# Optimization experiments

Hardware: AMD Instinct MI355X
Metric: run time of the kernel (lower is better)

The kernel has to match this reference:

```python
import jax, jax.numpy as jnp
import numpy as np
import itertools

B, H, W, C = 64, 28, 28, 576
NH, WS = 18, 7
KD = C // NH          # head dim = 32 (attn_ratio=1 so d == key_dim)
HID = 4 * C           # mlp hidden
N = WS * WS           # tokens per window = 49


def _bias_idxs():
    points = list(itertools.product(range(WS), range(WS)))
    offsets, idxs = {}, []
    for p1 in points:
        for p2 in points:
            off = (abs(p1[0] - p2[0]), abs(p1[1] - p2[1]))
            if off not in offsets:
                offsets[off] = len(offsets)
            idxs.append(offsets[off])
    return np.asarray(idxs, dtype=np.int64).reshape(N, N), len(offsets)


def setup_inputs() -> dict:
    key = jax.random.key(0)
    ks = jax.random.split(key, 10)
    idxs, n_off = _bias_idxs()  # n_off == 49
    s = 0.02
    return {
        "x": jax.random.normal(ks[0], (B, H * W, C), jnp.float32),
        "gamma_a": jnp.ones((C,), jnp.float32),
        "beta_a": jnp.zeros((C,), jnp.float32),
        "qkv_w": jax.random.normal(ks[1], (3 * C, C), jnp.float32) * s,
        "qkv_b": jnp.zeros((3 * C,), jnp.float32),
        "proj_w": jax.random.normal(ks[2], (C, C), jnp.float32) * s,
        "proj_b": jnp.zeros((C,), jnp.float32),
        "attn_biases": jax.random.normal(ks[3], (NH, n_off), jnp.float32) * s,
        "conv_w": jax.random.normal(ks[4], (C, 1, 3, 3), jnp.float32) * 0.1,
        "bn_gamma": jnp.ones((C,), jnp.float32),
        "bn_beta": jnp.zeros((C,), jnp.float32),
        "bn_mean": jnp.zeros((C,), jnp.float32),
        "bn_var": jax.random.uniform(ks[5], (C,), jnp.float32, 0.5, 1.5),
        "gamma_m": jnp.ones((C,), jnp.float32),
        "beta_m": jnp.zeros((C,), jnp.float32),
        "fc1_w": jax.random.normal(ks[6], (HID, C), jnp.float32) * s,
        "fc1_b": jnp.zeros((HID,), jnp.float32),
        "fc2_w": jax.random.normal(ks[7], (C, HID), jnp.float32) * s,
        "fc2_b": jnp.zeros((C,), jnp.float32),
        "bias_idxs": jnp.asarray(idxs),
    }


def _ln(x, g, b, eps=1e-5):
    mu = x.mean(-1, keepdims=True)
    var = ((x - mu) ** 2).mean(-1, keepdims=True)
    return (x - mu) * jax.lax.rsqrt(var + eps) * g + b


def reference(x, gamma_a, beta_a, qkv_w, qkv_b, proj_w, proj_b, attn_biases,
              conv_w, bn_gamma, bn_beta, bn_mean, bn_var,
              gamma_m, beta_m, fc1_w, fc1_b, fc2_w, fc2_b, bias_idxs):
    scale = KD ** -0.5
    nWh, nWw = H // WS, W // WS
    res = x
    # ---- window partition: (B, H*W, C) -> (B*nWh*nWw, 49, C) ----
    xw = x.reshape(B, nWh, WS, nWw, WS, C).transpose(0, 1, 3, 2, 4, 5)
    xw = xw.reshape(-1, N, C)
    # ---- windowed attention with gathered relative-position bias ----
    h = _ln(xw, gamma_a, beta_a)
    qkv = h @ qkv_w.T + qkv_b                       # (Bw, N, 3C)
    qkv = qkv.reshape(-1, N, NH, 3 * KD)
    q, k, v = jnp.split(qkv, 3, axis=-1)            # each (Bw, N, NH, KD)
    q = q.transpose(0, 2, 1, 3)
    k = k.transpose(0, 2, 1, 3)
    v = v.transpose(0, 2, 1, 3)
    bias = attn_biases[:, bias_idxs]                # (NH, N, N)
    attn = jnp.einsum('bhnd,bhmd->bhnm', q, k) * scale + bias
    attn = jax.nn.softmax(attn, axis=-1)
    out = jnp.einsum('bhnm,bhmd->bhnd', attn, v)    # (Bw, NH, N, KD)
    out = out.transpose(0, 2, 1, 3).reshape(-1, N, C) @ proj_w.T + proj_b
    # ---- window reverse ----
    out = out.reshape(B, nWh, nWw, WS, WS, C).transpose(0, 1, 3, 2, 4, 5)
    out = out.reshape(B, H * W, C)
    x = res + out
    # ---- depthwise 3x3 conv + BatchNorm (inference stats) ----
    xc = x.transpose(0, 2, 1).reshape(B, C, H, W)
    xc = jax.lax.conv_general_dilated(
        xc, conv_w, (1, 1), [(1, 1), (1, 1)],
        feature_group_count=C,
        dimension_numbers=('NCHW', 'OIHW', 'NCHW'))
    eps = 1e-5
    inv = (jax.lax.rsqrt(bn_var + eps) * bn_gamma)[:, None, None]
    xc = (xc - bn_mean[:, None, None]) * inv + bn_beta[:, None, None]
    x = xc.reshape(B, C, H * W).transpose(0, 2, 1)
    # ---- MLP with pre-LayerNorm ----
    hm = _ln(x, gamma_m, beta_m)
    hm = jax.nn.gelu(hm @ fc1_w.T + fc1_b, approximate=False)
    hm = hm @ fc2_w.T + fc2_b
    return x + hm
```

## Files before the change

kernel.cpp:

```cpp
#include <hip/hip_runtime.h>
#include <hip/hip_bf16.h>

typedef __bf16 v8bf  __attribute__((ext_vector_type(8)));
typedef __bf16 v4bf  __attribute__((ext_vector_type(4)));
typedef float  f32x4 __attribute__((ext_vector_type(4)));
typedef float  f32x8 __attribute__((ext_vector_type(8)));

#define TOKENS 50176
#define CDIM   576
#define NHEAD  18
#define QKVD   1728

__device__ __forceinline__ void gld16(const __bf16* g, __bf16* l)
{
    __builtin_amdgcn_global_load_lds(
        (const __attribute__((address_space(1))) void*)g,
        (__attribute__((address_space(3))) void*)l,
        16, 0, 0);
}

__device__ __forceinline__ float fast_gelu(float x)
{
    const float z  = x * 0.70710678118654752f;
    const float az = fabsf(z);
    const float t  = __frcp_rn(1.0f + 0.3275911f * az);
    float p = 1.061405429f;
    p = p * t - 1.453152027f;
    p = p * t + 1.421413741f;
    p = p * t - 0.284496736f;
    p = p * t + 0.254829592f;
    const float e   = __expf(-z * z);
    float erfv = 1.0f - p * t * e;
    erfv = copysignf(erfv, z);
    return 0.5f * x * (1.0f + erfv);
}

__global__ __launch_bounds__(256)
void cast_kernel(const float* __restrict__ in, __bf16* __restrict__ out)
{
    const size_t i = ((size_t)blockIdx.x * 256 + threadIdx.x) * 4;
    f32x4 v = *(const f32x4*)&in[i];
    v4bf o;
#pragma unroll
    for (int j = 0; j < 4; ++j) o[j] = (__bf16)v[j];
    *(v4bf*)&out[i] = o;
}

__global__ __launch_bounds__(64)
void conv_prep(const float* __restrict__ w, const float* __restrict__ bg,
               const float* __restrict__ bb, const float* __restrict__ bm,
               const float* __restrict__ bv, __bf16* __restrict__ wt,
               float* __restrict__ bias2)
{
    const int c = blockIdx.x * 64 + threadIdx.x;
    const float inv = rsqrtf(bv[c] + 1e-5f) * bg[c];
#pragma unroll
    for (int t = 0; t < 9; ++t) wt[t * CDIM + c] = (__bf16)(w[c * 9 + t] * inv);
    bias2[c] = bb[c] - bm[c] * inv;
}

template<typename InT>
__global__ __launch_bounds__(256)
void ln_kernel(const InT* __restrict__ x, const float* __restrict__ g,
               const float* __restrict__ b, __bf16* __restrict__ out)
{
    const int lane = threadIdx.x & 63;
    const int wid  = threadIdx.x >> 6;
    const size_t t = (size_t)blockIdx.x * 4 + wid;
    const InT* row = x + t * CDIM;

    float v[16];
    float sum = 0.f, sq = 0.f;
    if constexpr (sizeof(InT) == 2) {
        v8bf d0 = *(const v8bf*)&row[(size_t)lane * 8];
#pragma unroll
        for (int j = 0; j < 8; ++j) { float f = (float)d0[j]; v[j] = f; sum += f; sq += f * f; }
    } else {
        f32x8 d0 = *(const f32x8*)&row[(size_t)lane * 8];
#pragma unroll
        for (int j = 0; j < 8; ++j) { float f = d0[j]; v[j] = f; sum += f; sq += f * f; }
    }
    if (lane < 8) {
        if constexpr (sizeof(InT) == 2) {
            v8bf d1 = *(const v8bf*)&row[(size_t)(lane + 64) * 8];
#pragma unroll
            for (int j = 0; j < 8; ++j) { float f = (float)d1[j]; v[8 + j] = f; sum += f; sq += f * f; }
        } else {
            f32x8 d1 = *(const f32x8*)&row[(size_t)(lane + 64) * 8];
#pragma unroll
            for (int j = 0; j < 8; ++j) { float f = d1[j]; v[8 + j] = f; sum += f; sq += f * f; }
        }
    }
#pragma unroll
    for (int o = 32; o >= 1; o >>= 1) {
        sum += __shfl_xor(sum, o, 64);
        sq  += __shfl_xor(sq,  o, 64);
    }
    const float mean = sum * (1.0f / CDIM);
    const float rstd = rsqrtf(sq * (1.0f / CDIM) - mean * mean + 1e-5f);

    {
        int c0 = lane * 8;
        v8bf o0;
#pragma unroll
        for (int j = 0; j < 8; ++j)
            o0[j] = (__bf16)((v[j] - mean) * rstd * g[c0 + j] + b[c0 + j]);
        *(v8bf*)&out[t * CDIM + c0] = o0;
    }
    if (lane < 8) {
        int c0 = (lane + 64) * 8;
        v8bf o1;
#pragma unroll
        for (int j = 0; j < 8; ++j)
            o1[j] = (__bf16)((v[8 + j] - mean) * rstd * g[c0 + j] + b[c0 + j]);
        *(v8bf*)&out[t * CDIM + c0] = o1;
    }
}

template<int EPI, typename OutT, typename AddT>
__global__ __launch_bounds__(512, 1)
void gemm_bt(const __bf16* __restrict__ A, const __bf16* __restrict__ W,
             const float* __restrict__ bias, const AddT* __restrict__ add,
             OutT* __restrict__ C, int N, int K, int nN)
{
    constexpr int BM = 256, BN = 192, BK = 32;
    constexpr int ASZ = BM * BK;
    constexpr int BSZ = BN * BK;
    __shared__ __bf16 L[4][ASZ + BSZ];
    const int tid = threadIdx.x, lane = tid & 63, wid = tid >> 6;
    const int lr = lane & 15, kh = lane >> 4;
    const int wm = wid >> 2, wn = wid & 3;

    const int nwg = gridDim.x, bid = blockIdx.x;
    const int q = nwg >> 3, r = nwg & 7;
    const int xcd = bid & 7, jc = bid >> 3;
    const int wgid = (xcd < r ? xcd * (q + 1) : r * (q + 1) + (xcd - r) * q) + jc;
    const int mblk = wgid / nN, nblk = wgid - mblk * nN;
    const int m0 = mblk * BM, n0 = nblk * BN;

    const __bf16* pA = A + (size_t)(m0 + wid * 32 + lr) * K + kh * 8;
    const __bf16* pW = W + (size_t)(n0 + (wid < 6 ? wid : 0) * 32 + lr) * K + kh * 8;

    auto stageA = [&](int s, int kt) {
#pragma unroll
        for (int i = 0; i < 2; ++i)
            gld16(pA + (size_t)(i * 16) * K + kt * BK, &L[s][(wid * 2 + i) * 512]);
    };
    auto stageB = [&](int s, int kt) {
        if (wid < 6) {
#pragma unroll
            for (int i = 0; i < 2; ++i)
                gld16(pW + (size_t)(i * 16) * K + kt * BK,
                      &L[s][ASZ + (wid * 2 + i) * 512]);
        }
    };

    const int off = lane * 8;

    f32x4 acc[8][3] = {};
    const int NT = K / BK;

    stageA(0, 0); stageB(0, 0);
    stageA(1, 1); stageB(1, 1);

    for (int t = 0; t < NT; ++t) {
        if (t + 1 < NT) {
            if (wid < 6) asm volatile("s_waitcnt vmcnt(4)" ::: "memory");
            else         asm volatile("s_waitcnt vmcnt(2)" ::: "memory");
        } else {
            asm volatile("s_waitcnt vmcnt(0)" ::: "memory");
        }
        __builtin_amdgcn_s_barrier();

        const __bf16* Ls = L[t & 3];
        v8bf bfr[3], afr[4];

#pragma unroll
        for (int nf = 0; nf < 3; ++nf)
            bfr[nf] = *(const v8bf*)&Ls[ASZ + (wn * 3 + nf) * 512 + off];
#pragma unroll
        for (int mf = 0; mf < 4; ++mf)
            afr[mf] = *(const v8bf*)&Ls[(wm * 8 + mf) * 512 + off];

        if (t + 2 < NT) stageA((t + 2) & 3, t + 2);

        __builtin_amdgcn_s_setprio(1);
#pragma unroll
        for (int mf = 0; mf < 4; ++mf)
#pragma unroll
            for (int nf = 0; nf < 3; ++nf)
                acc[mf][nf] = __builtin_amdgcn_mfma_f32_16x16x32_bf16(
                    afr[mf], bfr[nf], acc[mf][nf], 0, 0, 0);
        __builtin_amdgcn_s_setprio(0);
        __builtin_amdgcn_s_barrier();

#pragma unroll
        for (int mf = 0; mf < 4; ++mf)
            afr[mf] = *(const v8bf*)&Ls[(wm * 8 + 4 + mf) * 512 + off];

        if (t + 2 < NT) stageB((t + 2) & 3, t + 2);

        __builtin_amdgcn_s_setprio(1);
#pragma unroll
        for (int mf = 0; mf < 4; ++mf)
#pragma unroll
            for (int nf = 0; nf < 3; ++nf)
                acc[4 + mf][nf] = __builtin_amdgcn_mfma_f32_16x16x32_bf16(
                    afr[mf], bfr[nf], acc[4 + mf][nf], 0, 0, 0);
        __builtin_amdgcn_s_setprio(0);
    }

#pragma unroll
    for (int mf = 0; mf < 8; ++mf)
#pragma unroll
        for (int nf = 0; nf < 3; ++nf)
#pragma unroll
            for (int rr = 0; rr < 4; ++rr) {
                int row = m0 + wm * 128 + mf * 16 + kh * 4 + rr;
                int col = n0 + wn * 48 + nf * 16 + lr;
                float vv = acc[mf][nf][rr] + bias[col];
                if (EPI == 1) vv += (float)add[(size_t)row * N + col];
                if (EPI == 2) vv = fast_gelu(vv);
                C[(size_t)row * N + col] = (OutT)vv;
            }
}

__global__ __launch_bounds__(64)
void attn_kernel(const __bf16* __restrict__ qkv, const float* __restrict__ biases,
                 const int* __restrict__ bidx, __bf16* __restrict__ out)
{
    const int head = blockIdx.x;
    const int win  = blockIdx.y;
    const int tid  = threadIdx.x;
    const int b  = win >> 4;
    const int wy = (win >> 2) & 3;
    const int wx = win & 3;
    __shared__ float kk[49][32];
    __shared__ float vv[49][32];
    const size_t hb = (size_t)head * 96;

    for (int e = tid; e < 49 * 32; e += 64) {
        int n = e >> 5, d = e & 31;
        int iy = n / 7, ix = n - iy * 7;
        size_t t = (size_t)b * 784 + (size_t)(wy * 7 + iy) * 28 + wx * 7 + ix;
        const __bf16* p = qkv + t * QKVD + hb;
        kk[n][d] = (float)p[32 + d];
        vv[n][d] = (float)p[64 + d];
    }
    float q[32];
    size_t tmine = 0;
    if (tid < 49) {
        int iy = tid / 7, ix = tid - iy * 7;
        tmine = (size_t)b * 784 + (size_t)(wy * 7 + iy) * 28 + wx * 7 + ix;
        const __bf16* p = qkv + tmine * QKVD + hb;
#pragma unroll
        for (int d = 0; d < 32; ++d) q[d] = (float)p[d];
    }
    __syncthreads();
    if (tid >= 49) return;

    const float scale = 0.17677669529663687f;
    float s[49];
    float mx = -1e30f;
    const int*   brow = bidx + tid * 49;
    const float* bh   = biases + head * 49;
#pragma unroll
    for (int m = 0; m < 49; ++m) {
        float dot = 0.f;
#pragma unroll
        for (int d = 0; d < 32; ++d) dot += q[d] * kk[m][d];
        float val = dot * scale + bh[brow[m]];
        s[m] = val;
        mx = fmaxf(mx, val);
    }
    float sum = 0.f;
#pragma unroll
    for (int m = 0; m < 49; ++m) { float e = __expf(s[m] - mx); s[m] = e; sum += e; }
    const float rs = 1.0f / sum;

    __bf16* op = out + tmine * CDIM + (size_t)head * 32;
#pragma unroll
    for (int d = 0; d < 32; ++d) {
        float a = 0.f;
#pragma unroll
        for (int m = 0; m < 49; ++m) a += s[m] * vv[m][d];
        op[d] = (__bf16)(a * rs);
    }
}

__global__ __launch_bounds__(256)
void conv_bn_v(const __bf16* __restrict__ xin, const __bf16* __restrict__ wt,
               const float* __restrict__ bias2, __bf16* __restrict__ xout)
{
    const size_t gt = (size_t)blockIdx.x * 256 + threadIdx.x;
    const int g = (int)(gt % 72);
    const size_t p = gt / 72;
    const int bimg = (int)(p / 784);
    const int pix  = (int)(p - (size_t)bimg * 784);
    const int y = pix / 28, xx = pix - y * 28;
    const int c0 = g * 8;

    float acc[8];
    {
        f32x4 b0 = *(const f32x4*)&bias2[c0];
        f32x4 b1 = *(const f32x4*)&bias2[c0 + 4];
#pragma unroll
        for (int jj = 0; jj < 4; ++jj) { acc[jj] = b0[jj]; acc[4 + jj] = b1[jj]; }
    }
#pragma unroll
    for (int dy = 0; dy < 3; ++dy) {
        int ny = y + dy - 1;
        if (ny < 0 || ny >= 28) continue;
#pragma unroll
        for (int dx = 0; dx < 3; ++dx) {
            int nx = xx + dx - 1;
            if (nx < 0 || nx >= 28) continue;
            v8bf xv = *(const v8bf*)&xin[((size_t)bimg * 784 + ny * 28 + nx) * CDIM + c0];
            v8bf wv = *(const v8bf*)&wt[(dy * 3 + dx) * CDIM + c0];
#pragma unroll
            for (int jj = 0; jj < 8; ++jj) acc[jj] += (float)xv[jj] * (float)wv[jj];
        }
    }
    v8bf o;
#pragma unroll
    for (int jj = 0; jj < 8; ++jj) o[jj] = (__bf16)acc[jj];
    *(v8bf*)&xout[p * CDIM + c0] = o;
}

extern "C" void kernel_launch(void* const* d_in, const int* in_sizes, int n_in,
                              void* d_out, int out_size, void* d_ws, size_t ws_size,
                              hipStream_t stream)
{
    (void)in_sizes; (void)n_in; (void)out_size; (void)ws_size;
    const float* x          = (const float*)d_in[0];
    const float* gamma_a    = (const float*)d_in[1];
    const float* beta_a     = (const float*)d_in[2];
    const float* qkv_w      = (const float*)d_in[3];
    const float* qkv_b      = (const float*)d_in[4];
    const float* proj_w     = (const float*)d_in[5];
    const float* proj_b     = (const float*)d_in[6];
    const float* attn_bias  = (const float*)d_in[7];
    const float* conv_w     = (const float*)d_in[8];
    const float* bn_g       = (const float*)d_in[9];
    const float* bn_b       = (const float*)d_in[10];
    const float* bn_m       = (const float*)d_in[11];
    const float* bn_v       = (const float*)d_in[12];
    const float* gamma_m    = (const float*)d_in[13];
    const float* beta_m     = (const float*)d_in[14];
    const float* fc1_w      = (const float*)d_in[15];
    const float* fc1_b      = (const float*)d_in[16];
    const float* fc2_w      = (const float*)d_in[17];
    const float* fc2_b      = (const float*)d_in[18];
    const int*   bidx       = (const int*)d_in[19];

    const size_t T = TOKENS;
    __bf16* ws     = (__bf16*)d_ws;
    __bf16* hbuf   = ws;
    __bf16* qkvbuf = ws + T * 576;
    __bf16* aout   = ws;
    __bf16* x2     = ws + T * 2304;
    __bf16* x3     = x2 + T * 576;
    __bf16* lnm    = x2;
    __bf16* f1     = ws;
    __bf16* wq     = x3 + T * 576;
    __bf16* wp     = wq + (size_t)QKVD * CDIM;
    __bf16* w1     = wp + (size_t)CDIM * CDIM;
    __bf16* w2     = w1 + (size_t)2304 * CDIM;
    __bf16* wt     = w2 + (size_t)CDIM * 2304;
    float*  bias2  = (float*)(wt + 9 * CDIM);
    float*  outp   = (float*)d_out;

    cast_kernel<<<dim3((QKVD * CDIM) / 1024), 256, 0, stream>>>(qkv_w, wq);
    cast_kernel<<<dim3((CDIM * CDIM) / 1024), 256, 0, stream>>>(proj_w, wp);
    cast_kernel<<<dim3((2304 * CDIM) / 1024), 256, 0, stream>>>(fc1_w, w1);
    cast_kernel<<<dim3((CDIM * 2304) / 1024), 256, 0, stream>>>(fc2_w, w2);
    conv_prep<<<dim3(9), 64, 0, stream>>>(conv_w, bn_g, bn_b, bn_m, bn_v, wt, bias2);

    ln_kernel<float><<<dim3(T / 4), 256, 0, stream>>>(x, gamma_a, beta_a, hbuf);
    gemm_bt<0, __bf16, float><<<dim3(196 * 9), 512, 0, stream>>>(
        hbuf, wq, qkv_b, nullptr, qkvbuf, QKVD, CDIM, 9);
    attn_kernel<<<dim3(NHEAD, 1024), 64, 0, stream>>>(qkvbuf, attn_bias, bidx, aout);
    gemm_bt<1, __bf16, float><<<dim3(196 * 3), 512, 0, stream>>>(
        aout, wp, proj_b, x, x2, CDIM, CDIM, 3);
    conv_bn_v<<<dim3(14112), 256, 0, stream>>>(x2, wt, bias2, x3);
    ln_kernel<__bf16><<<dim3(T / 4), 256, 0, stream>>>(x3, gamma_m, beta_m, lnm);
    gemm_bt<2, __bf16, float><<<dim3(196 * 12), 512, 0, stream>>>(
        lnm, w1, fc1_b, nullptr, f1, 2304, CDIM, 12);
    gemm_bt<1, float, __bf16><<<dim3(196 * 3), 512, 0, stream>>>(
        f1, w2, fc2_b, x3, outp, CDIM, 2304, 3);
}
```

Baseline: 1.021 ms.

## Rework GEMM to 4-wave 32x32x16 MFMA tiles with double buffering

Rewrites the shared GEMM kernel to use 256 threads (4 waves, 2x2 layout) with 32x32x16 bf16 MFMA instructions instead of 8 waves with 16x16x32, each wave now covering a 128x96 subtile. The LDS pipeline shrinks from a 4-stage to a 2-stage buffer with a full vmcnt(0) wait and barrier per k-step, and launch bounds allow two workgroups per CU. The aim is a higher MFMA-to-LDS-read ratio and better occupancy. The trade-off is a shallower prefetch that may expose global load latency, plus different register pressure.

```diff
diff --git a/kernel.cpp b/kernel.cpp
--- a/kernel.cpp
+++ b/kernel.cpp
@@ -5,6 +5,7 @@
 typedef __bf16 v4bf  __attribute__((ext_vector_type(4)));
 typedef float  f32x4 __attribute__((ext_vector_type(4)));
 typedef float  f32x8 __attribute__((ext_vector_type(8)));
+typedef float  f32x16 __attribute__((ext_vector_type(16)));
 
 #define TOKENS 50176
 #define CDIM   576
@@ -118,111 +119,118 @@
 }
 
 template<int EPI, typename OutT, typename AddT>
-__global__ __launch_bounds__(512, 1)
+__global__ __launch_bounds__(256, 2)
 void gemm_bt(const __bf16* __restrict__ A, const __bf16* __restrict__ W,
              const float* __restrict__ bias, const AddT* __restrict__ add,
              OutT* __restrict__ C, int N, int K, int nN)
 {
-    constexpr int BM = 256, BN = 192, BK = 32;
-    constexpr int ASZ = BM * BK;
-    constexpr int BSZ = BN * BK;
-    __shared__ __bf16 L[4][ASZ + BSZ];
+    constexpr int BK = 32;
+    constexpr int ASZ = 256 * BK;
+    constexpr int BSZ = 192 * BK;
+    __shared__ __bf16 L[2][ASZ + BSZ];
     const int tid = threadIdx.x, lane = tid & 63, wid = tid >> 6;
-    const int lr = lane & 15, kh = lane >> 4;
-    const int wm = wid >> 2, wn = wid & 3;
+    const int l31 = lane & 31, kg = lane >> 5;
+    const int wm = wid >> 1, wn = wid & 1;
 
     const int nwg = gridDim.x, bid = blockIdx.x;
     const int q = nwg >> 3, r = nwg & 7;
     const int xcd = bid & 7, jc = bid >> 3;
     const int wgid = (xcd < r ? xcd * (q + 1) : r * (q + 1) + (xcd - r) * q) + jc;
     const int mblk = wgid / nN, nblk = wgid - mblk * nN;
-    const int m0 = mblk * BM, n0 = nblk * BN;
-
-    const __bf16* pA = A + (size_t)(m0 + wid * 32 + lr) * K + kh * 8;
-    const __bf16* pW = W + (size_t)(n0 + (wid < 6 ? wid : 0) * 32 + lr) * K + kh * 8;
-
-    auto stageA = [&](int s, int kt) {
-#pragma unroll
-        for (int i = 0; i < 2; ++i)
-            gld16(pA + (size_t)(i * 16) * K + kt * BK, &L[s][(wid * 2 + i) * 512]);
+    const int m0 = mblk * 256, n0 = nblk * 192;
+
+    const __bf16* pAl = A + (size_t)(m0 + l31) * K + kg * 8;
+    const __bf16* pWl = W + (size_t)(n0 + l31) * K + kg * 8;
+
+    auto stage = [&](int s, int kt) {
+        const int kk = kt * BK;
+#pragma unroll
+        for (int i = 0; i < 7; ++i) {
+            const int e = wid + 4 * i;
+            if (e < 16) {
+                gld16(pAl + (size_t)((e >> 1) * 32) * K + kk + (e & 1) * 16,
+                      &L[s][e * 512]);
+            } else {
+                const int e2 = e - 16;
+                gld16(pWl + (size_t)((e2 >> 1) * 32) * K + kk + (e2 & 1) * 16,
+                      &L[s][ASZ + e2 * 512]);
+            }
+        }
     };
-    auto stageB = [&](int s, int kt) {
-        if (wid < 6) {
-#pragma unroll
-            for (int i = 0; i < 2; ++i)
-                gld16(pW + (size_t)(i * 16) * K + kt * BK,
-                      &L[s][ASZ + (wid * 2 + i) * 512]);
-        }
-    };
-
-    const int off = lane * 8;
-
-    f32x4 acc[8][3] = {};
+
+    const int lo = lane * 8;
+
+    f32x16 acc[4][3] = {};
     const int NT = K / BK;
 
-    stageA(0, 0); stageB(0, 0);
-    stageA(1, 1); stageB(1, 1);
-
+    stage(0, 0);
+    asm volatile("s_waitcnt vmcnt(0)" ::: "memory");
+    __builtin_amdgcn_s_barrier();
+
+    int cur = 0;
     for (int t = 0; t < NT; ++t) {
+        const __bf16* Ls = L[cur];
+        v8bf a0[4], b0[3];
+#pragma unroll
+        for (int mf = 0; mf < 4; ++mf)
+            a0[mf] = *(const v8bf*)&Ls[((wm * 4 + mf) * 2 + 0) * 512 + lo];
+#pragma unroll
+        for (int nf = 0; nf < 3; ++nf)
+            b0[nf] = *(const v8bf*)&Ls[ASZ + ((wn * 3 + nf) * 2 + 0) * 512 + lo];
+
+        if (t + 1 < NT) stage(cur ^ 1, t + 1);
+
+        __builtin_amdgcn_s_setprio(1);
+#pragma unroll
+        for (int mf = 0; mf < 4; ++mf)
+#pragma unroll
+            for (int nf = 0; nf < 3; ++nf)
+                acc[mf][nf] = __builtin_amdgcn_mfma_f32_32x32x16_bf16(
+                    a0[mf], b0[nf], acc[mf][nf], 0, 0, 0);
+        __builtin_amdgcn_s_setprio(0);
+
+        v8bf a1[4], b1[3];
+#pragma unroll
+        for (int mf = 0; mf < 4; ++mf)
+            a1[mf] = *(const v8bf*)&Ls[((wm * 4 + mf) * 2 + 1) * 512 + lo];
+#pragma unroll
+        for (int nf = 0; nf < 3; ++nf)
+            b1[nf] = *(const v8bf*)&Ls[ASZ + ((wn * 3 + nf) * 2 + 1) * 512 + lo];
+
+        __builtin_amdgcn_s_setprio(1);
+#pragma unroll
+        for (int mf = 0; mf < 4; ++mf)
+#pragma unroll
+            for (int nf = 0; nf < 3; ++nf)
+                acc[mf][nf] = __builtin_amdgcn_mfma_f32_32x32x16_bf16(
+                    a1[mf], b1[nf], acc[mf][nf], 0, 0, 0);
+        __builtin_amdgcn_s_setprio(0);
+
         if (t + 1 < NT) {
-            if (wid < 6) asm volatile("s_waitcnt vmcnt(4)" ::: "memory");
-            else         asm volatile("s_waitcnt vmcnt(2)" ::: "memory");
-        } else {
             asm volatile("s_waitcnt vmcnt(0)" ::: "memory");
-        }
-        __builtin_amdgcn_s_barrier();
-
-        const __bf16* Ls = L[t & 3];
-        v8bf bfr[3], afr[4];
-
-#pragma unroll
-        for (int nf = 0; nf < 3; ++nf)
-            bfr[nf] = *(const v8bf*)&Ls[ASZ + (wn * 3 + nf) * 512 + off];
-#pragma unroll
-        for (int mf = 0; mf < 4; ++mf)
-            afr[mf] = *(const v8bf*)&Ls[(wm * 8 + mf) * 512 + off];
-
-        if (t + 2 < NT) stageA((t + 2) & 3, t + 2);
-
-        __builtin_amdgcn_s_setprio(1);
-#pragma unroll
-        for (int mf = 0; mf < 4; ++mf)
-#pragma unroll
-            for (int nf = 0; nf < 3; ++nf)
-                acc[mf][nf] = __builtin_amdgcn_mfma_f32_16x16x32_bf16(
-                    afr[mf], bfr[nf], acc[mf][nf], 0, 0, 0);
-        __builtin_amdgcn_s_setprio(0);
-        __builtin_amdgcn_s_barrier();
-
-#pragma unroll
-        for (int mf = 0; mf < 4; ++mf)
-            afr[mf] = *(const v8bf*)&Ls[(wm * 8 + 4 + mf) * 512 + off];
-
-        if (t + 2 < NT) stageB((t + 2) & 3, t + 2);
-
-        __builtin_amdgcn_s_setprio(1);
-#pragma unroll
-        for (int mf = 0; mf < 4; ++mf)
-#pragma unroll
-            for (int nf = 0; nf < 3; ++nf)
-                acc[4 + mf][nf] = __builtin_amdgcn_mfma_f32_16x16x32_bf16(
-                    afr[mf], bfr[nf], acc[4 + mf][nf], 0, 0, 0);
-        __builtin_amdgcn_s_setprio(0);
-    }
-
-#pragma unroll
-    for (int mf = 0; mf < 8; ++mf)
-#pragma unroll
-        for (int nf = 0; nf < 3; ++nf)
-#pragma unroll
-            for (int rr = 0; rr < 4; ++rr) {
-                int row = m0 + wm * 128 + mf * 16 + kh * 4 + rr;
-                int col = n0 + wn * 48 + nf * 16 + lr;
-                float vv = acc[mf][nf][rr] + bias[col];
+            __builtin_amdgcn_s_barrier();
+            cur ^= 1;
+        }
+    }
+
+    float bc[3];
+#pragma unroll
+    for (int nf = 0; nf < 3; ++nf) bc[nf] = bias[n0 + wn * 96 + nf * 32 + l31];
+
+#pragma unroll
+    for (int mf = 0; mf < 4; ++mf)
+#pragma unroll
+        for (int nf = 0; nf < 3; ++nf) {
+            const int col = n0 + wn * 96 + nf * 32 + l31;
+#pragma unroll
+            for (int rr = 0; rr < 16; ++rr) {
+                const int row = m0 + wm * 128 + mf * 32 + (rr & 3) + 8 * (rr >> 2) + 4 * kg;
+                float vv = acc[mf][nf][rr] + bc[nf];
                 if (EPI == 1) vv += (float)add[(size_t)row * N + col];
                 if (EPI == 2) vv = fast_gelu(vv);
                 C[(size_t)row * N + col] = (OutT)vv;
             }
+        }
 }
 
 __global__ __launch_bounds__(64)
@@ -377,15 +385,15 @@
     conv_prep<<<dim3(9), 64, 0, stream>>>(conv_w, bn_g, bn_b, bn_m, bn_v, wt, bias2);
 
     ln_kernel<float><<<dim3(T / 4), 256, 0, stream>>>(x, gamma_a, beta_a, hbuf);
-    gemm_bt<0, __bf16, float><<<dim3(196 * 9), 512, 0, stream>>>(
+    gemm_bt<0, __bf16, float><<<dim3(196 * 9), 256, 0, stream>>>(
         hbuf, wq, qkv_b, nullptr, qkvbuf, QKVD, CDIM, 9);
     attn_kernel<<<dim3(NHEAD, 1024), 64, 0, stream>>>(qkvbuf, attn_bias, bidx, aout);
-    gemm_bt<1, __bf16, float><<<dim3(196 * 3), 512, 0, stream>>>(
+    gemm_bt<1, __bf16, float><<<dim3(196 * 3), 256, 0, stream>>>(
         aout, wp, proj_b, x, x2, CDIM, CDIM, 3);
     conv_bn_v<<<dim3(14112), 256, 0, stream>>>(x2, wt, bias2, x3);
     ln_kernel<__bf16><<<dim3(T / 4), 256, 0, stream>>>(x3, gamma_m, beta_m, lnm);
-    gemm_bt<2, __bf16, float><<<dim3(196 * 12), 512, 0, stream>>>(
+    gemm_bt<2, __bf16, float><<<dim3(196 * 12), 256, 0, stream>>>(
         lnm, w1, fc1_b, nullptr, f1, 2304, CDIM, 12);
-    gemm_bt<1, float, __bf16><<<dim3(196 * 3), 512, 0, stream>>>(
+    gemm_bt<1, float, __bf16><<<dim3(196 * 3), 256, 0, stream>>>(
         f1, w2, fc2_b, x3, outp, CDIM, 2304, 3);
 }
```

New measurement: 1.023 ms. About the same (+0.1%).

## Fuse depthwise conv+BN with MLP LayerNorm; use 128-row tiles for N=576 GEMMs

Applied to the files above, without the earlier changes.

The depthwise conv+BN kernel now also computes the MLP pre-LayerNorm, one wavefront per token, and writes both the residual x3 and the normalized input in one pass. This removes a separate LN kernel launch and a full re-read of x3. The GEMM is templated on BM, and the proj and fc2 GEMMs (N=576, only 3 column tiles) use BM=128, doubling the grid from 588 to 1176 workgroups to fill the GPU better. The risks are a conv that is less parallel per thread and smaller tiles with less reuse per workgroup.

```diff
diff --git a/kernel.cpp b/kernel.cpp
--- a/kernel.cpp
+++ b/kernel.cpp
@@ -59,37 +59,26 @@
     bias2[c] = bb[c] - bm[c] * inv;
 }
 
-template<typename InT>
 __global__ __launch_bounds__(256)
-void ln_kernel(const InT* __restrict__ x, const float* __restrict__ g,
+void ln_kernel(const float* __restrict__ x, const float* __restrict__ g,
                const float* __restrict__ b, __bf16* __restrict__ out)
 {
     const int lane = threadIdx.x & 63;
     const int wid  = threadIdx.x >> 6;
     const size_t t = (size_t)blockIdx.x * 4 + wid;
-    const InT* row = x + t * CDIM;
+    const float* row = x + t * CDIM;
 
     float v[16];
     float sum = 0.f, sq = 0.f;
-    if constexpr (sizeof(InT) == 2) {
-        v8bf d0 = *(const v8bf*)&row[(size_t)lane * 8];
-#pragma unroll
-        for (int j = 0; j < 8; ++j) { float f = (float)d0[j]; v[j] = f; sum += f; sq += f * f; }
-    } else {
+    {
         f32x8 d0 = *(const f32x8*)&row[(size_t)lane * 8];
 #pragma unroll
         for (int j = 0; j < 8; ++j) { float f = d0[j]; v[j] = f; sum += f; sq += f * f; }
     }
     if (lane < 8) {
-        if constexpr (sizeof(InT) == 2) {
-            v8bf d1 = *(const v8bf*)&row[(size_t)(lane + 64) * 8];
-#pragma unroll
-            for (int j = 0; j < 8; ++j) { float f = (float)d1[j]; v[8 + j] = f; sum += f; sq += f * f; }
-        } else {
-            f32x8 d1 = *(const f32x8*)&row[(size_t)(lane + 64) * 8];
-#pragma unroll
-            for (int j = 0; j < 8; ++j) { float f = d1[j]; v[8 + j] = f; sum += f; sq += f * f; }
-        }
+        f32x8 d1 = *(const f32x8*)&row[(size_t)(lane + 64) * 8];
+#pragma unroll
+        for (int j = 0; j < 8; ++j) { float f = d1[j]; v[8 + j] = f; sum += f; sq += f * f; }
     }
 #pragma unroll
     for (int o = 32; o >= 1; o >>= 1) {
@@ -117,15 +106,17 @@
     }
 }
 
-template<int EPI, typename OutT, typename AddT>
+template<int BM, int EPI, typename OutT, typename AddT>
 __global__ __launch_bounds__(512, 1)
 void gemm_bt(const __bf16* __restrict__ A, const __bf16* __restrict__ W,
              const float* __restrict__ bias, const AddT* __restrict__ add,
              OutT* __restrict__ C, int N, int K, int nN)
 {
-    constexpr int BM = 256, BN = 192, BK = 32;
+    constexpr int BK  = 32;
     constexpr int ASZ = BM * BK;
-    constexpr int BSZ = BN * BK;
+    constexpr int BSZ = 192 * BK;
+    constexpr int MFR = BM / 32;
+    constexpr int MH  = MFR / 2;
     __shared__ __bf16 L[4][ASZ + BSZ];
     const int tid = threadIdx.x, lane = tid & 63, wid = tid >> 6;
     const int lr = lane & 15, kh = lane >> 4;
@@ -136,15 +127,21 @@
     const int xcd = bid & 7, jc = bid >> 3;
     const int wgid = (xcd < r ? xcd * (q + 1) : r * (q + 1) + (xcd - r) * q) + jc;
     const int mblk = wgid / nN, nblk = wgid - mblk * nN;
-    const int m0 = mblk * BM, n0 = nblk * BN;
-
-    const __bf16* pA = A + (size_t)(m0 + wid * 32 + lr) * K + kh * 8;
+    const int m0 = mblk * BM, n0 = nblk * 192;
+
+    const __bf16* pA;
+    if constexpr (BM == 256) pA = A + (size_t)(m0 + wid * 32 + lr) * K + kh * 8;
+    else                     pA = A + (size_t)(m0 + wid * 16 + lr) * K + kh * 8;
     const __bf16* pW = W + (size_t)(n0 + (wid < 6 ? wid : 0) * 32 + lr) * K + kh * 8;
 
     auto stageA = [&](int s, int kt) {
-#pragma unroll
-        for (int i = 0; i < 2; ++i)
-            gld16(pA + (size_t)(i * 16) * K + kt * BK, &L[s][(wid * 2 + i) * 512]);
+        if constexpr (BM == 256) {
+#pragma unroll
+            for (int i = 0; i < 2; ++i)
+                gld16(pA + (size_t)(i * 16) * K + kt * BK, &L[s][(wid * 2 + i) * 512]);
+        } else {
+            gld16(pA + kt * BK, &L[s][wid * 512]);
+        }
     };
     auto stageB = [&](int s, int kt) {
         if (wid < 6) {
@@ -155,9 +152,9 @@
         }
     };
 
-    const int off = lane * 8;
-
-    f32x4 acc[8][3] = {};
+    const int lo = lane * 8;
+
+    f32x4 acc[MFR][3] = {};
     const int NT = K / BK;
 
     stageA(0, 0); stageB(0, 0);
@@ -165,28 +162,33 @@
 
     for (int t = 0; t < NT; ++t) {
         if (t + 1 < NT) {
-            if (wid < 6) asm volatile("s_waitcnt vmcnt(4)" ::: "memory");
-            else         asm volatile("s_waitcnt vmcnt(2)" ::: "memory");
+            if constexpr (BM == 256) {
+                if (wid < 6) asm volatile("s_waitcnt vmcnt(4)" ::: "memory");
+                else         asm volatile("s_waitcnt vmcnt(2)" ::: "memory");
+            } else {
+                if (wid < 6) asm volatile("s_waitcnt vmcnt(3)" ::: "memory");
+                else         asm volatile("s_waitcnt vmcnt(1)" ::: "memory");
+            }
         } else {
             asm volatile("s_waitcnt vmcnt(0)" ::: "memory");
         }
         __builtin_amdgcn_s_barrier();
 
         const __bf16* Ls = L[t & 3];
-        v8bf bfr[3], afr[4];
+        v8bf bfr[3], afr[MH];
 
 #pragma unroll
         for (int nf = 0; nf < 3; ++nf)
-            bfr[nf] = *(const v8bf*)&Ls[ASZ + (wn * 3 + nf) * 512 + off];
-#pragma unroll
-        for (int mf = 0; mf < 4; ++mf)
-            afr[mf] = *(const v8bf*)&Ls[(wm * 8 + mf) * 512 + off];
+            bfr[nf] = *(const v8bf*)&Ls[ASZ + (wn * 3 + nf) * 512 + lo];
+#pragma unroll
+        for (int mf = 0; mf < MH; ++mf)
+            afr[mf] = *(const v8bf*)&Ls[(wm * MFR + mf) * 512 + lo];
 
         if (t + 2 < NT) stageA((t + 2) & 3, t + 2);
 
         __builtin_amdgcn_s_setprio(1);
 #pragma unroll
-        for (int mf = 0; mf < 4; ++mf)
+        for (int mf = 0; mf < MH; ++mf)
 #pragma unroll
             for (int nf = 0; nf < 3; ++nf)
                 acc[mf][nf] = __builtin_amdgcn_mfma_f32_16x16x32_bf16(
@@ -195,28 +197,28 @@
         __builtin_amdgcn_s_barrier();
 
 #pragma unroll
-        for (int mf = 0; mf < 4; ++mf)
-            afr[mf] = *(const v8bf*)&Ls[(wm * 8 + 4 + mf) * 512 + off];
+        for (int mf = 0; mf < MH; ++mf)
+            afr[mf] = *(const v8bf*)&Ls[(wm * MFR + MH + mf) * 512 + lo];
 
         if (t + 2 < NT) stageB((t + 2) & 3, t + 2);
 
         __builtin_amdgcn_s_setprio(1);
 #pragma unroll
-        for (int mf = 0; mf < 4; ++mf)
+        for (int mf = 0; mf < MH; ++mf)
 #pragma unroll
             for (int nf = 0; nf < 3; ++nf)
-                acc[4 + mf][nf] = __builtin_amdgcn_mfma_f32_16x16x32_bf16(
-                    afr[mf], bfr[nf], acc[4 + mf][nf], 0, 0, 0);
+                acc[MH + mf][nf] = __builtin_amdgcn_mfma_f32_16x16x32_bf16(
+                    afr[mf], bfr[nf], acc[MH + mf][nf], 0, 0, 0);
         __builtin_amdgcn_s_setprio(0);
     }
 
 #pragma unroll
-    for (int mf = 0; mf < 8; ++mf)
+    for (int mf = 0; mf < MFR; ++mf)
 #pragma unroll
         for (int nf = 0; nf < 3; ++nf)
 #pragma unroll
             for (int rr = 0; rr < 4; ++rr) {
-                int row = m0 + wm * 128 + mf * 16 + kh * 4 + rr;
+                int row = m0 + wm * (BM / 2) + mf * 16 + kh * 4 + rr;
                 int col = n0 + wn * 48 + nf * 16 + lr;
                 float vv = acc[mf][nf][rr] + bias[col];
                 if (EPI == 1) vv += (float)add[(size_t)row * N + col];
@@ -289,42 +291,101 @@
 }
 
 __global__ __launch_bounds__(256)
-void conv_bn_v(const __bf16* __restrict__ xin, const __bf16* __restrict__ wt,
-               const float* __restrict__ bias2, __bf16* __restrict__ xout)
-{
-    const size_t gt = (size_t)blockIdx.x * 256 + threadIdx.x;
-    const int g = (int)(gt % 72);
-    const size_t p = gt / 72;
+void conv_bn_ln(const __bf16* __restrict__ xin, const __bf16* __restrict__ wt,
+                const float* __restrict__ bias2, const float* __restrict__ g,
+                const float* __restrict__ b,
+                __bf16* __restrict__ x3, __bf16* __restrict__ lnm)
+{
+    const int lane = threadIdx.x & 63;
+    const int wid  = threadIdx.x >> 6;
+    const size_t p = (size_t)blockIdx.x * 4 + wid;
     const int bimg = (int)(p / 784);
     const int pix  = (int)(p - (size_t)bimg * 784);
     const int y = pix / 28, xx = pix - y * 28;
-    const int c0 = g * 8;
-
-    float acc[8];
+    const size_t rowbase = (size_t)bimg * 784;
+
+    float v[16];
+    float sum = 0.f, sq = 0.f;
+
     {
+        const int c0 = lane * 8;
+        float a[8];
         f32x4 b0 = *(const f32x4*)&bias2[c0];
         f32x4 b1 = *(const f32x4*)&bias2[c0 + 4];
 #pragma unroll
-        for (int jj = 0; jj < 4; ++jj) { acc[jj] = b0[jj]; acc[4 + jj] = b1[jj]; }
-    }
-#pragma unroll
-    for (int dy = 0; dy < 3; ++dy) {
-        int ny = y + dy - 1;
-        if (ny < 0 || ny >= 28) continue;
-#pragma unroll
-        for (int dx = 0; dx < 3; ++dx) {
-            int nx = xx + dx - 1;
-            if (nx < 0 || nx >= 28) continue;
-            v8bf xv = *(const v8bf*)&xin[((size_t)bimg * 784 + ny * 28 + nx) * CDIM + c0];
-            v8bf wv = *(const v8bf*)&wt[(dy * 3 + dx) * CDIM + c0];
-#pragma unroll
-            for (int jj = 0; jj < 8; ++jj) acc[jj] += (float)xv[jj] * (float)wv[jj];
-        }
-    }
-    v8bf o;
-#pragma unroll
-    for (int jj = 0; jj < 8; ++jj) o[jj] = (__bf16)acc[jj];
-    *(v8bf*)&xout[p * CDIM + c0] = o;
+        for (int j = 0; j < 4; ++j) { a[j] = b0[j]; a[4 + j] = b1[j]; }
+#pragma unroll
+        for (int dy = 0; dy < 3; ++dy) {
+            int ny = y + dy - 1;
+            if (ny < 0 || ny >= 28) continue;
+#pragma unroll
+            for (int dx = 0; dx < 3; ++dx) {
+                int nx = xx + dx - 1;
+                if (nx < 0 || nx >= 28) continue;
+                v8bf xv = *(const v8bf*)&xin[(rowbase + ny * 28 + nx) * CDIM + c0];
+                v8bf wv = *(const v8bf*)&wt[(dy * 3 + dx) * CDIM + c0];
+#pragma unroll
+                for (int j = 0; j < 8; ++j) a[j] += (float)xv[j] * (float)wv[j];
+            }
+        }
+#pragma unroll
+        for (int j = 0; j < 8; ++j) { v[j] = a[j]; sum += a[j]; sq += a[j] * a[j]; }
+    }
+    if (lane < 8) {
+        const int c0 = 512 + lane * 8;
+        float a[8];
+        f32x4 b0 = *(const f32x4*)&bias2[c0];
+        f32x4 b1 = *(const f32x4*)&bias2[c0 + 4];
+#pragma unroll
+        for (int j = 0; j < 4; ++j) { a[j] = b0[j]; a[4 + j] = b1[j]; }
+#pragma unroll
+        for (int dy = 0; dy < 3; ++dy) {
+            int ny = y + dy - 1;
+            if (ny < 0 || ny >= 28) continue;
+#pragma unroll
+            for (int dx = 0; dx < 3; ++dx) {
+                int nx = xx + dx - 1;
+                if (nx < 0 || nx >= 28) continue;
+                v8bf xv = *(const v8bf*)&xin[(rowbase + ny * 28 + nx) * CDIM + c0];
+                v8bf wv = *(const v8bf*)&wt[(dy * 3 + dx) * CDIM + c0];
+#pragma unroll
+                for (int j = 0; j < 8; ++j) a[j] += (float)xv[j] * (float)wv[j];
+            }
+        }
+#pragma unroll
+        for (int j = 0; j < 8; ++j) { v[8 + j] = a[j]; sum += a[j]; sq += a[j] * a[j]; }
+    }
+
+#pragma unroll
+    for (int o = 32; o >= 1; o >>= 1) {
+        sum += __shfl_xor(sum, o, 64);
+        sq  += __shfl_xor(sq,  o, 64);
+    }
+    const float mean = sum * (1.0f / CDIM);
+    const float rstd = rsqrtf(sq * (1.0f / CDIM) - mean * mean + 1e-5f);
+
+    {
+        const int c0 = lane * 8;
+        v8bf o3, ol;
+#pragma unroll
+        for (int j = 0; j < 8; ++j) {
+            o3[j] = (__bf16)v[j];
+            ol[j] = (__bf16)((v[j] - mean) * rstd * g[c0 + j] + b[c0 + j]);
+        }
+        *(v8bf*)&x3[p * CDIM + c0]  = o3;
+        *(v8bf*)&lnm[p * CDIM + c0] = ol;
+    }
+    if (lane < 8) {
+        const int c0 = 512 + lane * 8;
+        v8bf o3, ol;
+#pragma unroll
+        for (int j = 0; j < 8; ++j) {
+            o3[j] = (__bf16)v[8 + j];
+            ol[j] = (__bf16)((v[8 + j] - mean) * rstd * g[c0 + j] + b[c0 + j]);
+        }
+        *(v8bf*)&x3[p * CDIM + c0]  = o3;
+        *(v8bf*)&lnm[p * CDIM + c0] = ol;
+    }
 }
 
 extern "C" void kernel_launch(void* const* d_in, const int* in_sizes, int n_in,
@@ -359,9 +420,9 @@
     __bf16* qkvbuf = ws + T * 576;
     __bf16* aout   = ws;
     __bf16* x2     = ws + T * 2304;
-    __bf16* x3     = x2 + T * 576;
-    __bf16* lnm    = x2;
-    __bf16* f1     = ws;
+    __bf16* x3     = ws + T * 2880;
+    __bf16* lnm    = ws;
+    __bf16* f1     = ws + T * 576;
     __bf16* wq     = x3 + T * 576;
     __bf16* wp     = wq + (size_t)QKVD * CDIM;
     __bf16* w1     = wp + (size_t)CDIM * CDIM;
@@ -376,16 +437,16 @@
     cast_kernel<<<dim3((CDIM * 2304) / 1024), 256, 0, stream>>>(fc2_w, w2);
     conv_prep<<<dim3(9), 64, 0, stream>>>(conv_w, bn_g, bn_b, bn_m, bn_v, wt, bias2);
 
-    ln_kernel<float><<<dim3(T / 4), 256, 0, stream>>>(x, gamma_a, beta_a, hbuf);
-    gemm_bt<0, __bf16, float><<<dim3(196 * 9), 512, 0, stream>>>(
+    ln_kernel<<<dim3(T / 4), 256, 0, stream>>>(x, gamma_a, beta_a, hbuf);
+    gemm_bt<256, 0, __bf16, float><<<dim3(196 * 9), 512, 0, stream>>>(
         hbuf, wq, qkv_b, nullptr, qkvbuf, QKVD, CDIM, 9);
     attn_kernel<<<dim3(NHEAD, 1024), 64, 0, stream>>>(qkvbuf, attn_bias, bidx, aout);
-    gemm_bt<1, __bf16, float><<<dim3(196 * 3), 512, 0, stream>>>(
+    gemm_bt<128, 1, __bf16, float><<<dim3(392 * 3), 512, 0, stream>>>(
         aout, wp, proj_b, x, x2, CDIM, CDIM, 3);
-    conv_bn_v<<<dim3(14112), 256, 0, stream>>>(x2, wt, bias2, x3);
-    ln_kernel<__bf16><<<dim3(T / 4), 256, 0, stream>>>(x3, gamma_m, beta_m, lnm);
-    gemm_bt<2, __bf16, float><<<dim3(196 * 12), 512, 0, stream>>>(
+    conv_bn_ln<<<dim3(12544), 256, 0, stream>>>(x2, wt, bias2, gamma_m, beta_m,
+                                                x3, lnm);
+    gemm_bt<256, 2, __bf16, float><<<dim3(196 * 12), 512, 0, stream>>>(
         lnm, w1, fc1_b, nullptr, f1, 2304, CDIM, 12);
-    gemm_bt<1, float, __bf16><<<dim3(196 * 3), 512, 0, stream>>>(
+    gemm_bt<128, 1, float, __bf16><<<dim3(392 * 3), 512, 0, stream>>>(
         f1, w2, fc2_b, x3, outp, CDIM, 2304, 3);
 }
```

Result: slower. 1.054 ms (+3.2%).
